# Kernel tuning notes

Hardware: AMD Instinct MI355X
Metric: run time of the kernel (lower is better)

## Reference

```python
import jax, jax.numpy as jnp
import numpy as np

CAR_DIM = 8
ESC_MAX_AGENT = 32
HID = 256
ACTION_DIM = 30
NUM_STATES = 64
BATCH = 8192
ENC_OUT = 1 + CAR_DIM * ESC_MAX_AGENT          # 257
Q_IN = 1 + CAR_DIM + CAR_DIM * ESC_MAX_AGENT   # 265


def setup_inputs() -> dict:
    key = jax.random.key(0)
    ks = jax.random.split(key, 9)
    s = jax.random.normal(ks[0], (BATCH, CAR_DIM + NUM_STATES * CAR_DIM), dtype=jnp.float32)
    def lin(k, fan_in, fan_out):
        bound = 1.0 / np.sqrt(fan_in)
        kw, kb = jax.random.split(k)
        W = jax.random.uniform(kw, (fan_in, fan_out), jnp.float32, -bound, bound)
        b = jax.random.uniform(kb, (fan_out,), jnp.float32, -bound, bound)
        return W, b
    W1, b1 = lin(ks[1], CAR_DIM, HID)
    W2, b2 = lin(ks[2], HID, ENC_OUT)
    Qw1, Qb1 = lin(ks[3], Q_IN, HID)
    Qw2, Qb2 = lin(ks[4], HID, ACTION_DIM)
    return {"s": s, "W1": W1, "b1": b1, "W2": W2, "b2": b2,
            "Qw1": Qw1, "Qb1": Qb1, "Qw2": Qw2, "Qb2": Qb2}


def reference(s, W1, b1, W2, b2, Qw1, Qb1, Qw2, Qb2):
    B = s.shape[0]
    self_states = s[:, :CAR_DIM]                                   # [B, C]
    surr = s[:, CAR_DIM:].reshape(B, -1, CAR_DIM)                  # [B, N, C]
    # sentinel agents: any coordinate exactly == -1 is skipped
    valid = ~jnp.any(surr == -1.0, axis=-1)                        # [B, N] bool
    h = jax.nn.relu(jnp.einsum('bnc,ch->bnh', surr, W1) + b1)      # [B, N, HID]
    enc = jax.nn.relu(jnp.einsum('bnh,he->bne', h, W2) + b2)       # [B, N, ENC_OUT]
    sum_outputs = jnp.sum(enc * valid[:, :, None].astype(enc.dtype), axis=1)  # [B, ENC_OUT]
    x = jnp.concatenate([self_states, sum_outputs], axis=1)        # [B, Q_IN]
    q = jax.nn.relu(x @ Qw1 + Qb1) @ Qw2 + Qb2                     # [B, ACTION_DIM]
    return q
```

## Files before the change

kernel.cpp:

```cpp
#include <hip/hip_runtime.h>

#define CAR 8
#define SROW 520
#define HID 256
#define EOUT 257
#define XPAD 288
#define ADIM 30

typedef __attribute__((ext_vector_type(8))) short sh8;
typedef __attribute__((ext_vector_type(4))) float f32x4;

__device__ __forceinline__ short f2bf(float f) {
  unsigned u = __builtin_bit_cast(unsigned, f);
  u += 0x7fffu + ((u >> 16) & 1u);
  return (short)(u >> 16);
}
__device__ __forceinline__ unsigned f2bf2(float a, float b) {
  unsigned ua = __builtin_bit_cast(unsigned, a);
  ua += 0x7fffu + ((ua >> 16) & 1u);
  unsigned ub = __builtin_bit_cast(unsigned, b);
  ub += 0x7fffu + ((ub >> 16) & 1u);
  return __builtin_amdgcn_perm(ub, ua, 0x07060302);
}
__device__ __forceinline__ unsigned pkt(float a, float b) {
  return __builtin_amdgcn_perm(__builtin_bit_cast(unsigned, b),
                               __builtin_bit_cast(unsigned, a), 0x07060302);
}

__global__ void k_prep(const float* __restrict__ W1, const float* __restrict__ b1,
                       const float* __restrict__ W2,
                       const float* __restrict__ Qw1, const float* __restrict__ Qw2,
                       short* __restrict__ w1f, short* __restrict__ w2f,
                       short* __restrict__ w3f, short* __restrict__ wq2f) {
  int idx = blockIdx.x * 256 + threadIdx.x;
  if (idx < 8192) {
    int mt = idx >> 9, r = idx & 511, lane = r >> 3, j = r & 7;
    int quad = lane >> 4, m = lane & 15;
    int hid = mt * 16 + m;
    float v = (quad == 0) ? W1[j * HID + hid]
            : (quad == 1 && j == 0) ? b1[hid] : 0.0f;
    w1f[idx] = f2bf(v);
    return;
  }
  int i2 = idx - 8192;
  if (i2 < 69632) {
    int ks = i2 / 8704, r = i2 % 8704;
    int nt = r >> 9, r2 = r & 511, lane = r2 >> 3, j = r2 & 7;
    int quad = lane >> 4, m = lane & 15;
    int k = ks * 32 + quad * 8 + j, n = nt * 16 + m;
    float v = (n < EOUT) ? W2[k * EOUT + n] : 0.0f;
    w2f[i2] = f2bf(v);
    return;
  }
  int i3 = i2 - 69632;
  if (i3 < 73728) {
    int ks = i3 >> 13, r = i3 & 8191;
    int nt = r >> 9, r2 = r & 511, lane = r2 >> 3, j = r2 & 7;
    int quad = lane >> 4, m = lane & 15;
    int k = ks * 32 + quad * 8 + j, n = nt * 16 + m;
    float v = (k < 265) ? Qw1[k * HID + n] : 0.0f;
    w3f[i3] = f2bf(v);
    return;
  }
  int i4 = i3 - 73728;
  if (i4 < 8192) {
    int ks = i4 >> 10, r = i4 & 1023;
    int nt = r >> 9, r2 = r & 511, lane = r2 >> 3, j = r2 & 7;
    int quad = lane >> 4, m = lane & 15;
    int k = ks * 32 + quad * 8 + j, n = nt * 16 + m;
    float v = (n < ADIM) ? Qw2[k * ADIM + n] : 0.0f;
    wq2f[i4] = f2bf(v);
  }
}

__global__ __launch_bounds__(256, 4)
void k_enc(const float* __restrict__ s, const short* __restrict__ w1f,
           const short* __restrict__ w2f, const float* __restrict__ b2,
           float* __restrict__ so288, int B) {
  __shared__ __align__(16) short hlds[16384];
  __shared__ float ninvp[4];
  __shared__ float t16[4][16];

  const int tid = threadIdx.x;
  const int w = tid >> 6, lane = tid & 63;
  const int q = lane >> 4, m = lane & 15;
  const size_t bg = blockIdx.x;

  const float* srow0 = s + bg * SROW + CAR;
  int4 pk = {0, 0, 0, 0};
  bool inv = false;
  if (lane < 16) {
    const float* sr = srow0 + (w * 16 + lane) * CAR;
    float4 f0 = ((const float4*)sr)[0], f1 = ((const float4*)sr)[1];
    inv = (f0.x == -1.f) | (f0.y == -1.f) | (f0.z == -1.f) | (f0.w == -1.f) |
          (f1.x == -1.f) | (f1.y == -1.f) | (f1.z == -1.f) | (f1.w == -1.f);
    if (!inv) {
      pk.x = (int)f2bf2(f0.x, f0.y); pk.y = (int)f2bf2(f0.z, f0.w);
      pk.z = (int)f2bf2(f1.x, f1.y); pk.w = (int)f2bf2(f1.z, f1.w);
    }
  }
  const float vflag = inv ? 0.f : 1.f;
  unsigned long long bal = __ballot(inv);
  if (lane == 0) ninvp[w] = (float)__popcll(bal);

  if (w == 1) {
    if (lane < CAR)       so288[bg * XPAD + lane] = s[bg * SROW + lane];
    else if (lane < 16)   so288[bg * XPAD + 280 + (lane - 8)] = 0.f;
  }

  int4 p0;
  p0.x = __shfl(pk.x, m, 64); p0.y = __shfl(pk.y, m, 64);
  p0.z = __shfl(pk.z, m, 64); p0.w = __shfl(pk.w, m, 64);
  const float vv0 = __shfl(vflag, m, 64);
  if (q == 1) {
    p0.x = (vv0 != 0.f) ? 0x3f80 : 0; p0.y = p0.z = p0.w = 0;
  } else if (q >= 2) {
    p0.x = p0.y = p0.z = p0.w = 0;
  }
  sh8 bs = __builtin_bit_cast(sh8, p0);

#pragma unroll 4
  for (int mt = 0; mt < 16; ++mt) {
    sh8 af = *(const sh8*)(w1f + (mt * 64 + lane) * 8);
    f32x4 z = {0.f, 0.f, 0.f, 0.f};
    f32x4 c0 = __builtin_amdgcn_mfma_f32_16x16x32_bf16(af, bs, z, 0, 0, 0);
    const int hidb = mt * 16 + q * 4;
    const int ks = hidb >> 5, qB = (hidb >> 3) & 3, js = hidb & 7;
    uint2 k0;
    k0.x = pkt(fmaxf(c0[0], 0.f), fmaxf(c0[1], 0.f));
    k0.y = pkt(fmaxf(c0[2], 0.f), fmaxf(c0[3], 0.f));
    *(uint2*)(&hlds[((w * 8 + ks) * 64 + qB * 16 + m) * 8 + js]) = k0;
  }
  __syncthreads();

  f32x4 acc[4][4];
  f32x4 acc16 = {0.f, 0.f, 0.f, 0.f};
#pragma unroll
  for (int mtA = 0; mtA < 4; ++mtA)
#pragma unroll
    for (int i = 0; i < 4; ++i) {
      f32x4 z = {0.f, 0.f, 0.f, 0.f};
      acc[mtA][i] = z;
    }
  const int t0 = 4 * w;
#pragma unroll 2
  for (int ks = 0; ks < 8; ++ks) {
    sh8 A0 = *(const sh8*)(&hlds[((0 * 8 + ks) * 64 + lane) * 8]);
    sh8 A1 = *(const sh8*)(&hlds[((1 * 8 + ks) * 64 + lane) * 8]);
    sh8 A2 = *(const sh8*)(&hlds[((2 * 8 + ks) * 64 + lane) * 8]);
    sh8 A3 = *(const sh8*)(&hlds[((3 * 8 + ks) * 64 + lane) * 8]);
    sh8 A16 = *(const sh8*)(&hlds[((w * 8 + ks) * 64 + lane) * 8]);
#pragma unroll
    for (int i = 0; i < 4; ++i) {
      sh8 Bf = *(const sh8*)(w2f + ((ks * 17 + t0 + i) * 64 + lane) * 8);
      acc[0][i] = __builtin_amdgcn_mfma_f32_16x16x32_bf16(A0, Bf, acc[0][i], 0, 0, 0);
      acc[1][i] = __builtin_amdgcn_mfma_f32_16x16x32_bf16(A1, Bf, acc[1][i], 0, 0, 0);
      acc[2][i] = __builtin_amdgcn_mfma_f32_16x16x32_bf16(A2, Bf, acc[2][i], 0, 0, 0);
      acc[3][i] = __builtin_amdgcn_mfma_f32_16x16x32_bf16(A3, Bf, acc[3][i], 0, 0, 0);
    }
    sh8 B16 = *(const sh8*)(w2f + ((ks * 17 + 16) * 64 + lane) * 8);
    acc16 = __builtin_amdgcn_mfma_f32_16x16x32_bf16(A16, B16, acc16, 0, 0, 0);
  }

  const float ninv = ninvp[0] + ninvp[1] + ninvp[2] + ninvp[3];
#pragma unroll
  for (int i = 0; i < 4; ++i) {
    const int col = (t0 + i) * 16 + m;
    const float b2c = b2[col];
    float ssum = 0.f;
#pragma unroll
    for (int mtA = 0; mtA < 4; ++mtA)
#pragma unroll
      for (int r = 0; r < 4; ++r)
        ssum += fmaxf(acc[mtA][i][r] + b2c, 0.f);
    ssum += __shfl_xor(ssum, 16, 64);
    ssum += __shfl_xor(ssum, 32, 64);
    ssum -= ninv * fmaxf(b2c, 0.f);
    if (q == 0) so288[bg * XPAD + CAR + col] = ssum;
  }
  {
    const int colc = 256 + m;
    const float b2c = (colc < EOUT) ? b2[colc] : 0.f;
    float s16 = 0.f;
#pragma unroll
    for (int r = 0; r < 4; ++r)
      s16 += fmaxf(acc16[r] + b2c, 0.f);
    s16 += __shfl_xor(s16, 16, 64);
    s16 += __shfl_xor(s16, 32, 64);
    if (q == 0) t16[w][m] = s16;
  }
  __syncthreads();
  if (w == 0 && q == 0) {
    const int colc = 256 + m;
    const float b2c = (colc < EOUT) ? b2[colc] : 0.f;
    const float tot = t16[0][m] + t16[1][m] + t16[2][m] + t16[3][m]
                    - ninv * fmaxf(b2c, 0.f);
    so288[bg * XPAD + CAR + colc] = tot;
  }
}

__global__ __launch_bounds__(256, 2)
void k_q(const float* __restrict__ so288, const short* __restrict__ w3f,
         const float* __restrict__ Qb1, const short* __restrict__ wq2f,
         const float* __restrict__ Qb2, float* __restrict__ out, int B) {
  __shared__ __align__(16) short xf[2 * 9 * 64 * 8];
  __shared__ __align__(16) float H[32 * 260];
  const int tid = threadIdx.x;
  const int w = tid >> 6, lane = tid & 63;
  const int q = lane >> 4, m = lane & 15;
  const int b0 = blockIdx.x * 32;

#pragma unroll
  for (int it = 0; it < 5; ++it) {
    int sidx = tid + it * 256;
    if (sidx < 1152) {
      int mt = sidx / 576, rem = sidx % 576;
      int ks = rem >> 6, l = rem & 63;
      int lq = l >> 4, lm = l & 15;
      int row = b0 + mt * 16 + lm; if (row >= B) row = B - 1;
      const float* xp = so288 + (size_t)row * XPAD + ks * 32 + lq * 8;
      float4 xa = ((const float4*)xp)[0], xb = ((const float4*)xp)[1];
      int4 t = {(int)f2bf2(xa.x, xa.y), (int)f2bf2(xa.z, xa.w),
                (int)f2bf2(xb.x, xb.y), (int)f2bf2(xb.z, xb.w)};
      *(int4*)(xf + sidx * 8) = t;
    }
  }
  __syncthreads();

  f32x4 acc1[2][4];
#pragma unroll
  for (int mt = 0; mt < 2; ++mt)
#pragma unroll
    for (int i = 0; i < 4; ++i) {
      f32x4 z = {0.f, 0.f, 0.f, 0.f};
      acc1[mt][i] = z;
    }
#pragma unroll
  for (int ks = 0; ks < 9; ++ks) {
    sh8 A0 = *(const sh8*)(xf + ((0 * 9 + ks) * 64 + lane) * 8);
    sh8 A1 = *(const sh8*)(xf + ((1 * 9 + ks) * 64 + lane) * 8);
#pragma unroll
    for (int i = 0; i < 4; ++i) {
      sh8 Bf = *(const sh8*)(w3f + ((ks * 16 + 4 * w + i) * 64 + lane) * 8);
      acc1[0][i] = __builtin_amdgcn_mfma_f32_16x16x32_bf16(A0, Bf, acc1[0][i], 0, 0, 0);
      acc1[1][i] = __builtin_amdgcn_mfma_f32_16x16x32_bf16(A1, Bf, acc1[1][i], 0, 0, 0);
    }
  }
#pragma unroll
  for (int i = 0; i < 4; ++i) {
    const int hcol = (4 * w + i) * 16 + m;
    const float bq = Qb1[hcol];
#pragma unroll
    for (int mt = 0; mt < 2; ++mt)
#pragma unroll
      for (int r = 0; r < 4; ++r)
        H[(mt * 16 + q * 4 + r) * 260 + hcol] = fmaxf(acc1[mt][i][r] + bq, 0.f);
  }
  __syncthreads();

  const int mt2 = w >> 1, nt2 = w & 1;
  f32x4 acc2 = {0.f, 0.f, 0.f, 0.f};
#pragma unroll
  for (int ks = 0; ks < 8; ++ks) {
    const float* hp = H + (mt2 * 16 + m) * 260 + ks * 32 + q * 8;
    float4 ha = ((const float4*)hp)[0], hb = ((const float4*)hp)[1];
    int4 t = {(int)f2bf2(ha.x, ha.y), (int)f2bf2(ha.z, ha.w),
              (int)f2bf2(hb.x, hb.y), (int)f2bf2(hb.z, hb.w)};
    sh8 A2 = __builtin_bit_cast(sh8, t);
    sh8 Bf = *(const sh8*)(wq2f + ((ks * 2 + nt2) * 64 + lane) * 8);
    acc2 = __builtin_amdgcn_mfma_f32_16x16x32_bf16(A2, Bf, acc2, 0, 0, 0);
  }
  const int act = nt2 * 16 + m;
  if (act < ADIM) {
    const float bq = Qb2[act];
#pragma unroll
    for (int r = 0; r < 4; ++r) {
      const int row = b0 + mt2 * 16 + q * 4 + r;
      if (row < B) out[(size_t)row * ADIM + act] = acc2[r] + bq;
    }
  }
}

extern "C" void kernel_launch(void* const* d_in, const int* in_sizes, int n_in,
                              void* d_out, int out_size, void* d_ws, size_t ws_size,
                              hipStream_t stream) {
  const float* s   = (const float*)d_in[0];
  const float* W1  = (const float*)d_in[1];
  const float* b1  = (const float*)d_in[2];
  const float* W2  = (const float*)d_in[3];
  const float* b2  = (const float*)d_in[4];
  const float* Qw1 = (const float*)d_in[5];
  const float* Qb1 = (const float*)d_in[6];
  const float* Qw2 = (const float*)d_in[7];
  const float* Qb2 = (const float*)d_in[8];
  float* out = (float*)d_out;
  const int B = in_sizes[0] / SROW;

  char* wsb = (char*)d_ws;
  float* so288 = (float*)wsb;
  size_t off = (size_t)B * XPAD * sizeof(float);
  short* w1f  = (short*)(wsb + off);            off += 8192 * 2;
  short* w2f  = (short*)(wsb + off);            off += 69632 * 2;
  short* w3f  = (short*)(wsb + off);            off += 73728 * 2;
  short* wq2f = (short*)(wsb + off);

  const int prep_elems = 8192 + 69632 + 73728 + 8192;
  k_prep<<<(prep_elems + 255) / 256, 256, 0, stream>>>(W1, b1, W2, Qw1, Qw2,
                                                       w1f, w2f, w3f, wq2f);
  k_enc<<<B, 256, 0, stream>>>(s, w1f, w2f, b2, so288, B);
  k_q<<<(B + 31) / 32, 256, 0, stream>>>(so288, w3f, Qb1, wq2f, Qb2, out, B);
}
```

Measured before the change: 173.9 us.

## Process two batch rows per encoder block to share W2 fragment loads

The encoder kernel now runs 512-thread blocks that each handle two batch rows, with each wave owning two output column tiles across both rows instead of four tiles for one row. Each W2 B-fragment loaded from global memory is reused for MFMAs on both rows, halving W2 traffic per row, and the grid size is halved. This costs doubled LDS for the hidden activations, more accumulator pressure per wave, and clamping logic for an odd batch tail.

```diff
diff --git a/kernel.cpp b/kernel.cpp
--- a/kernel.cpp
+++ b/kernel.cpp
@@ -73,24 +73,26 @@
   }
 }
 
-__global__ __launch_bounds__(256, 4)
+__global__ __launch_bounds__(512, 4)
 void k_enc(const float* __restrict__ s, const short* __restrict__ w1f,
            const short* __restrict__ w2f, const float* __restrict__ b2,
            float* __restrict__ so288, int B) {
-  __shared__ __align__(16) short hlds[16384];
-  __shared__ float ninvp[4];
-  __shared__ float t16[4][16];
+  __shared__ __align__(16) short hlds[2][16384];
+  __shared__ float ninvp[8];
+  __shared__ float t16[8][16];
 
   const int tid = threadIdx.x;
   const int w = tid >> 6, lane = tid & 63;
   const int q = lane >> 4, m = lane & 15;
-  const size_t bg = blockIdx.x;
+  const int we = w >> 2, g = w & 3;
+  const size_t bg0 = 2 * (size_t)blockIdx.x;
+  size_t bg = bg0 + we; if (bg >= (size_t)B) bg = B - 1;
 
   const float* srow0 = s + bg * SROW + CAR;
   int4 pk = {0, 0, 0, 0};
   bool inv = false;
   if (lane < 16) {
-    const float* sr = srow0 + (w * 16 + lane) * CAR;
+    const float* sr = srow0 + (g * 16 + lane) * CAR;
     float4 f0 = ((const float4*)sr)[0], f1 = ((const float4*)sr)[1];
     inv = (f0.x == -1.f) | (f0.y == -1.f) | (f0.z == -1.f) | (f0.w == -1.f) |
           (f1.x == -1.f) | (f1.y == -1.f) | (f1.z == -1.f) | (f1.w == -1.f);
@@ -103,9 +105,10 @@
   unsigned long long bal = __ballot(inv);
   if (lane == 0) ninvp[w] = (float)__popcll(bal);
 
-  if (w == 1) {
-    if (lane < CAR)       so288[bg * XPAD + lane] = s[bg * SROW + lane];
-    else if (lane < 16)   so288[bg * XPAD + 280 + (lane - 8)] = 0.f;
+  if (w == 1 || w == 2) {
+    size_t rr = bg0 + (w - 1); if (rr >= (size_t)B) rr = B - 1;
+    if (lane < CAR)       so288[rr * XPAD + lane] = s[rr * SROW + lane];
+    else if (lane < 16)   so288[rr * XPAD + 280 + (lane - 8)] = 0.f;
   }
 
   int4 p0;
@@ -129,54 +132,69 @@
     uint2 k0;
     k0.x = pkt(fmaxf(c0[0], 0.f), fmaxf(c0[1], 0.f));
     k0.y = pkt(fmaxf(c0[2], 0.f), fmaxf(c0[3], 0.f));
-    *(uint2*)(&hlds[((w * 8 + ks) * 64 + qB * 16 + m) * 8 + js]) = k0;
+    *(uint2*)(&hlds[we][((g * 8 + ks) * 64 + qB * 16 + m) * 8 + js]) = k0;
   }
   __syncthreads();
 
-  f32x4 acc[4][4];
+  f32x4 acc[4][2][2];
   f32x4 acc16 = {0.f, 0.f, 0.f, 0.f};
 #pragma unroll
   for (int mtA = 0; mtA < 4; ++mtA)
 #pragma unroll
-    for (int i = 0; i < 4; ++i) {
-      f32x4 z = {0.f, 0.f, 0.f, 0.f};
-      acc[mtA][i] = z;
-    }
-  const int t0 = 4 * w;
-#pragma unroll 2
+    for (int i = 0; i < 2; ++i)
+#pragma unroll
+      for (int e = 0; e < 2; ++e) {
+        f32x4 z = {0.f, 0.f, 0.f, 0.f};
+        acc[mtA][i][e] = z;
+      }
+  const int t0 = 2 * w;
+#pragma unroll
   for (int ks = 0; ks < 8; ++ks) {
-    sh8 A0 = *(const sh8*)(&hlds[((0 * 8 + ks) * 64 + lane) * 8]);
-    sh8 A1 = *(const sh8*)(&hlds[((1 * 8 + ks) * 64 + lane) * 8]);
-    sh8 A2 = *(const sh8*)(&hlds[((2 * 8 + ks) * 64 + lane) * 8]);
-    sh8 A3 = *(const sh8*)(&hlds[((3 * 8 + ks) * 64 + lane) * 8]);
-    sh8 A16 = *(const sh8*)(&hlds[((w * 8 + ks) * 64 + lane) * 8]);
-#pragma unroll
-    for (int i = 0; i < 4; ++i) {
-      sh8 Bf = *(const sh8*)(w2f + ((ks * 17 + t0 + i) * 64 + lane) * 8);
-      acc[0][i] = __builtin_amdgcn_mfma_f32_16x16x32_bf16(A0, Bf, acc[0][i], 0, 0, 0);
-      acc[1][i] = __builtin_amdgcn_mfma_f32_16x16x32_bf16(A1, Bf, acc[1][i], 0, 0, 0);
-      acc[2][i] = __builtin_amdgcn_mfma_f32_16x16x32_bf16(A2, Bf, acc[2][i], 0, 0, 0);
-      acc[3][i] = __builtin_amdgcn_mfma_f32_16x16x32_bf16(A3, Bf, acc[3][i], 0, 0, 0);
-    }
-    sh8 B16 = *(const sh8*)(w2f + ((ks * 17 + 16) * 64 + lane) * 8);
+    sh8 B0  = *(const sh8*)(w2f + ((ks * 17 + t0)     * 64 + lane) * 8);
+    sh8 B1  = *(const sh8*)(w2f + ((ks * 17 + t0 + 1) * 64 + lane) * 8);
+    sh8 B16 = *(const sh8*)(w2f + ((ks * 17 + 16)     * 64 + lane) * 8);
+    sh8 A16 = *(const sh8*)(&hlds[we][((g * 8 + ks) * 64 + lane) * 8]);
     acc16 = __builtin_amdgcn_mfma_f32_16x16x32_bf16(A16, B16, acc16, 0, 0, 0);
-  }
-
-  const float ninv = ninvp[0] + ninvp[1] + ninvp[2] + ninvp[3];
-#pragma unroll
-  for (int i = 0; i < 4; ++i) {
+#pragma unroll
+    for (int e = 0; e < 2; ++e) {
+      sh8 A0 = *(const sh8*)(&hlds[e][((0 * 8 + ks) * 64 + lane) * 8]);
+      sh8 A1 = *(const sh8*)(&hlds[e][((1 * 8 + ks) * 64 + lane) * 8]);
+      sh8 A2 = *(const sh8*)(&hlds[e][((2 * 8 + ks) * 64 + lane) * 8]);
+      sh8 A3 = *(const sh8*)(&hlds[e][((3 * 8 + ks) * 64 + lane) * 8]);
+      acc[0][0][e] = __builtin_amdgcn_mfma_f32_16x16x32_bf16(A0, B0, acc[0][0][e], 0, 0, 0);
+      acc[1][0][e] = __builtin_amdgcn_mfma_f32_16x16x32_bf16(A1, B0, acc[1][0][e], 0, 0, 0);
+      acc[2][0][e] = __builtin_amdgcn_mfma_f32_16x16x32_bf16(A2, B0, acc[2][0][e], 0, 0, 0);
+      acc[3][0][e] = __builtin_amdgcn_mfma_f32_16x16x32_bf16(A3, B0, acc[3][0][e], 0, 0, 0);
+      acc[0][1][e] = __builtin_amdgcn_mfma_f32_16x16x32_bf16(A0, B1, acc[0][1][e], 0, 0, 0);
+      acc[1][1][e] = __builtin_amdgcn_mfma_f32_16x16x32_bf16(A1, B1, acc[1][1][e], 0, 0, 0);
+      acc[2][1][e] = __builtin_amdgcn_mfma_f32_16x16x32_bf16(A2, B1, acc[2][1][e], 0, 0, 0);
+      acc[3][1][e] = __builtin_amdgcn_mfma_f32_16x16x32_bf16(A3, B1, acc[3][1][e], 0, 0, 0);
+    }
+  }
+
+  const float ninv[2] = {ninvp[0] + ninvp[1] + ninvp[2] + ninvp[3],
+                         ninvp[4] + ninvp[5] + ninvp[6] + ninvp[7]};
+#pragma unroll
+  for (int i = 0; i < 2; ++i) {
     const int col = (t0 + i) * 16 + m;
     const float b2c = b2[col];
-    float ssum = 0.f;
-#pragma unroll
-    for (int mtA = 0; mtA < 4; ++mtA)
-#pragma unroll
-      for (int r = 0; r < 4; ++r)
-        ssum += fmaxf(acc[mtA][i][r] + b2c, 0.f);
-    ssum += __shfl_xor(ssum, 16, 64);
-    ssum += __shfl_xor(ssum, 32, 64);
-    ssum -= ninv * fmaxf(b2c, 0.f);
-    if (q == 0) so288[bg * XPAD + CAR + col] = ssum;
+    const float rb2 = fmaxf(b2c, 0.f);
+#pragma unroll
+    for (int e = 0; e < 2; ++e) {
+      float ssum = 0.f;
+#pragma unroll
+      for (int mtA = 0; mtA < 4; ++mtA)
+#pragma unroll
+        for (int r = 0; r < 4; ++r)
+          ssum += fmaxf(acc[mtA][i][e][r] + b2c, 0.f);
+      ssum += __shfl_xor(ssum, 16, 64);
+      ssum += __shfl_xor(ssum, 32, 64);
+      ssum -= ninv[e] * rb2;
+      if (q == 0) {
+        size_t rr = bg0 + e; if (rr >= (size_t)B) rr = B - 1;
+        so288[rr * XPAD + CAR + col] = ssum;
+      }
+    }
   }
   {
     const int colc = 256 + m;
@@ -190,12 +208,15 @@
     if (q == 0) t16[w][m] = s16;
   }
   __syncthreads();
-  if (w == 0 && q == 0) {
+  if ((w == 0 || w == 4) && q == 0) {
+    const int e = w >> 2;
     const int colc = 256 + m;
     const float b2c = (colc < EOUT) ? b2[colc] : 0.f;
-    const float tot = t16[0][m] + t16[1][m] + t16[2][m] + t16[3][m]
-                    - ninv * fmaxf(b2c, 0.f);
-    so288[bg * XPAD + CAR + colc] = tot;
+    const float tot = t16[e * 4 + 0][m] + t16[e * 4 + 1][m] +
+                      t16[e * 4 + 2][m] + t16[e * 4 + 3][m]
+                    - ninv[e] * fmaxf(b2c, 0.f);
+    size_t rr = bg0 + e; if (rr >= (size_t)B) rr = B - 1;
+    so288[rr * XPAD + CAR + colc] = tot;
   }
 }
 
@@ -307,6 +328,6 @@
   const int prep_elems = 8192 + 69632 + 73728 + 8192;
   k_prep<<<(prep_elems + 255) / 256, 256, 0, stream>>>(W1, b1, W2, Qw1, Qw2,
                                                        w1f, w2f, w3f, wq2f);
-  k_enc<<<B, 256, 0, stream>>>(s, w1f, w2f, b2, so288, B);
+  k_enc<<<(B + 1) / 2, 512, 0, stream>>>(s, w1f, w2f, b2, so288, B);
   k_q<<<(B + 31) / 32, 256, 0, stream>>>(so288, w3f, Qb1, wq2f, Qb2, out, B);
 }
```

Result: faster. 160.6 us (-7.7%).
